# Performance work log

Hardware: AMD Instinct MI355X
Metric: run time of the kernel (lower is better)

## Reference

```python
import jax, jax.numpy as jnp
import numpy as np

EMB = 1024
HEADS = 16
B, N = 2, 2048

def setup_inputs() -> dict:
    key = jax.random.key(0)
    ks = jax.random.split(key, 9)
    s = 1.0 / np.sqrt(EMB)
    return {
        "x": jax.random.normal(ks[0], (B, N, EMB), dtype=jnp.float32),
        "Wq": jax.random.normal(ks[1], (EMB, EMB), dtype=jnp.float32) * s,
        "bq": jax.random.normal(ks[2], (EMB,), dtype=jnp.float32) * 0.01,
        "Wk": jax.random.normal(ks[3], (EMB, EMB), dtype=jnp.float32) * s,
        "bk": jax.random.normal(ks[4], (EMB,), dtype=jnp.float32) * 0.01,
        "Wv": jax.random.normal(ks[5], (EMB, EMB), dtype=jnp.float32) * s,
        "bv": jax.random.normal(ks[6], (EMB,), dtype=jnp.float32) * 0.01,
        "Wo": jax.random.normal(ks[7], (EMB, EMB), dtype=jnp.float32) * s,
        "bo": jax.random.normal(ks[8], (EMB,), dtype=jnp.float32) * 0.01,
    }

def _split_heads(t):
    b, n, e = t.shape
    return t.reshape(b, n, HEADS, e // HEADS).transpose(0, 2, 1, 3)  # b h n d

def reference(x, Wq, bq, Wk, bk, Wv, bv, Wo, bo):
    q = _split_heads(x @ Wq + bq)
    k = _split_heads(x @ Wk + bk)
    v = _split_heads(x @ Wv + bv)
    # NOTE: original scales by sqrt(emb_size), not sqrt(head_dim)
    scaling = jnp.asarray(EMB, x.dtype) ** 0.5
    energy = jnp.einsum('bhqd,bhkd->bhqk', q, k)
    att = jax.nn.softmax(energy / scaling, axis=-1)
    out = jnp.einsum('bhqk,bhkd->bhqd', att, v)
    out = out.transpose(0, 2, 1, 3).reshape(x.shape[0], x.shape[1], EMB)
    return out @ Wo + bo
```

## Files before the change

### kernel.cpp

```cpp
#include <hip/hip_runtime.h>
#include <hip/hip_bf16.h>

typedef __bf16 bf16_t;
typedef bf16_t bf16x8 __attribute__((ext_vector_type(8)));
typedef float f32x4 __attribute__((ext_vector_type(4)));
typedef float f32x2 __attribute__((ext_vector_type(2)));
typedef float f32x16 __attribute__((ext_vector_type(16)));

#define EMB 1024
#define HEADS 16
#define BATCH 2
#define SEQ 2048
#define HD 64
#define TOKENS (BATCH * SEQ)

__device__ __forceinline__ void gld16(bf16_t* lds_dst, const bf16_t* g_src) {
    __builtin_amdgcn_global_load_lds(
        (const __attribute__((address_space(1))) unsigned int*)g_src,
        (__attribute__((address_space(3))) unsigned int*)lds_dst, 16, 0, 0);
}

__device__ __forceinline__ unsigned cvt_pk_bf16(float lo, float hi) {
    unsigned r;
    asm("v_cvt_pk_bf16_f32 %0, %1, %2" : "=v"(r) : "v"(lo), "v"(hi));
    return r;
}

__device__ __forceinline__ float exp2_fast(float x) {
#if __has_builtin(__builtin_amdgcn_exp2f)
    return __builtin_amdgcn_exp2f(x);
#else
    return __expf(x * 0.69314718056f);
#endif
}

#define WAITV(N) asm volatile("s_waitcnt vmcnt(" #N ")" ::: "memory")
#define WAITLGKM() asm volatile("s_waitcnt lgkmcnt(0)" ::: "memory")
#define BAR() __builtin_amdgcn_s_barrier()

__global__ __launch_bounds__(256) void prep_all(
    const float* __restrict__ x, bf16_t* __restrict__ xb,
    const float* __restrict__ W0, const float* __restrict__ W1,
    const float* __restrict__ W2, const float* __restrict__ W3,
    bf16_t* __restrict__ T0, bf16_t* __restrict__ T1,
    bf16_t* __restrict__ T2, bf16_t* __restrict__ T3) {
    __shared__ __align__(16) bf16_t T[64][72];
    if (blockIdx.x < 1024) {
        size_t i = ((size_t)blockIdx.x * 256 + threadIdx.x) * 16;
        f32x4 v0 = *(const f32x4*)&x[i];
        f32x4 v1 = *(const f32x4*)&x[i + 4];
        f32x4 v2 = *(const f32x4*)&x[i + 8];
        f32x4 v3 = *(const f32x4*)&x[i + 12];
        bf16x8 o0, o1;
#pragma unroll
        for (int j = 0; j < 4; ++j) {
            o0[j] = (bf16_t)v0[j]; o0[4 + j] = (bf16_t)v1[j];
            o1[j] = (bf16_t)v2[j]; o1[4 + j] = (bf16_t)v3[j];
        }
        *(bf16x8*)&xb[i] = o0;
        *(bf16x8*)&xb[i + 8] = o1;
        return;
    }
    int t = blockIdx.x - 1024;
    int z = t >> 8, rid = t & 255;
    const float* src = (z == 0) ? W0 : (z == 1) ? W1 : (z == 2) ? W2 : W3;
    bf16_t* dst = (z == 0) ? T0 : (z == 1) ? T1 : (z == 2) ? T2 : T3;
    int k0 = (rid >> 4) * 64, n0 = (rid & 15) * 64;
    int r = threadIdx.x >> 2, c4 = (threadIdx.x & 3) * 16;
    f32x4 v[4];
#pragma unroll
    for (int q = 0; q < 4; ++q)
        v[q] = *(const f32x4*)&src[(size_t)(k0 + r) * 1024 + n0 + c4 + q * 4];
#pragma unroll
    for (int j = 0; j < 16; ++j) T[c4 + j][r] = (bf16_t)v[j >> 2][j & 3];
    __syncthreads();
    bf16x8 o0 = *(const bf16x8*)&T[r][c4];
    bf16x8 o1 = *(const bf16x8*)&T[r][c4 + 8];
    *(bf16x8*)&dst[(size_t)(n0 + r) * 1024 + k0 + c4] = o0;
    *(bf16x8*)&dst[(size_t)(n0 + r) * 1024 + k0 + c4 + 8] = o1;
}

template <typename TO>
__global__ __launch_bounds__(512) void gemm8p(
    const bf16_t* __restrict__ A, const bf16_t* __restrict__ W,
    const float* __restrict__ b0, const float* __restrict__ b1, const float* __restrict__ b2,
    TO* __restrict__ o0, TO* __restrict__ o1, TO* __restrict__ o2,
    int md0, int md1, int md2, float sc0, float sc1, float sc2,
    int XMP, int XNP, int CXM, int CXS) {
    __shared__ __align__(16) bf16_t As[2][256 * 64];
    __shared__ __align__(16) bf16_t Bs[2][256 * 64];

    const int tid = threadIdx.x, w = tid >> 6, lane = tid & 63;
    const int quad = lane >> 4, cc = lane & 15;
    const int wr = w >> 2, wc = w & 3;

    const int lin = blockIdx.x;
    const int xc = lin & 7, t = lin >> 3;
    const int mi = (xc & CXM) * XMP + (t % XMP);
    const int ni = (xc >> CXS) * XNP + (t / XMP);
    const int m0 = mi * 256, n0 = ni * 256;

    const int z = n0 >> 10;
    const float* bias = (z == 0) ? b0 : (z == 1) ? b1 : b2;
    TO* out = (z == 0) ? o0 : (z == 1) ? o1 : o2;
    const int mode = (z == 0) ? md0 : (z == 1) ? md1 : md2;
    const float scale = (z == 0) ? sc0 : (z == 1) ? sc1 : sc2;
    const int nz = n0 & 1023;

    f32x4 acc[8][4];
#pragma unroll
    for (int i = 0; i < 8; ++i)
#pragma unroll
        for (int j = 0; j < 4; ++j) acc[i][j] = (f32x4){0.f, 0.f, 0.f, 0.f};

    const int r8 = lane >> 3, sg = lane & 7;
    const int g8 = (sg ^ r8) * 8;
    const bf16_t* Ag = A + (size_t)m0 * 1024;
    const bf16_t* Bg = W + (size_t)n0 * 1024;

#define ST_A(BUF, TILE, H)                                                     \
    {                                                                          \
        _Pragma("unroll")                                                      \
        for (int s = 0; s < 2; ++s) {                                          \
            int rg = (H) * 128 + (w * 2 + s) * 8;                              \
            gld16(&As[BUF][rg * 64],                                           \
                  &Ag[(size_t)(rg + r8) * 1024 + (TILE) * 64 + g8]);           \
        }                                                                      \
    }
#define ST_B(BUF, TILE, H)                                                     \
    {                                                                          \
        _Pragma("unroll")                                                      \
        for (int s = 0; s < 2; ++s) {                                          \
            int rg = (H) * 128 + (w * 2 + s) * 8;                              \
            gld16(&Bs[BUF][rg * 64],                                           \
                  &Bg[(size_t)(rg + r8) * 1024 + (TILE) * 64 + g8]);           \
        }                                                                      \
    }

    const int soq = (quad ^ (cc & 7)) * 8;
    int rArow[8], rBrow[4];
#pragma unroll
    for (int mt = 0; mt < 8; ++mt) rArow[mt] = (wr * 128 + mt * 16 + cc) * 64;
#pragma unroll
    for (int nt = 0; nt < 4; ++nt) rBrow[nt] = (wc * 64 + nt * 16 + cc) * 64;

    bf16x8 bfr[4][2];
#define RD_B(BUF)                                                              \
    {                                                                          \
        _Pragma("unroll")                                                      \
        for (int nt = 0; nt < 4; ++nt) {                                       \
            bfr[nt][0] = *(const bf16x8*)&Bs[BUF][rBrow[nt] + soq];            \
            bfr[nt][1] = *(const bf16x8*)&Bs[BUF][rBrow[nt] + (soq ^ 32)];     \
        }                                                                      \
    }

#define PHASE(BUF, Q, STG)                                                     \
    {                                                                          \
        bf16x8 af0a = *(const bf16x8*)&As[BUF][rArow[(Q) * 2] + soq];          \
        bf16x8 af0b = *(const bf16x8*)&As[BUF][rArow[(Q) * 2] + (soq ^ 32)];   \
        bf16x8 af1a = *(const bf16x8*)&As[BUF][rArow[(Q) * 2 + 1] + soq];      \
        bf16x8 af1b = *(const bf16x8*)&As[BUF][rArow[(Q) * 2 + 1] + (soq ^ 32)]; \
        STG;                                                                   \
        WAITLGKM();                                                            \
        __builtin_amdgcn_sched_barrier(0);                                     \
        __builtin_amdgcn_s_setprio(1);                                         \
        _Pragma("unroll")                                                      \
        for (int nt = 0; nt < 4; ++nt) {                                       \
            acc[(Q) * 2][nt] = __builtin_amdgcn_mfma_f32_16x16x32_bf16(        \
                af0a, bfr[nt][0], acc[(Q) * 2][nt], 0, 0, 0);                  \
            acc[(Q) * 2][nt] = __builtin_amdgcn_mfma_f32_16x16x32_bf16(        \
                af0b, bfr[nt][1], acc[(Q) * 2][nt], 0, 0, 0);                  \
            acc[(Q) * 2 + 1][nt] = __builtin_amdgcn_mfma_f32_16x16x32_bf16(    \
                af1a, bfr[nt][0], acc[(Q) * 2 + 1][nt], 0, 0, 0);              \
            acc[(Q) * 2 + 1][nt] = __builtin_amdgcn_mfma_f32_16x16x32_bf16(    \
                af1b, bfr[nt][1], acc[(Q) * 2 + 1][nt], 0, 0, 0);              \
        }                                                                      \
        __builtin_amdgcn_s_setprio(0);                                         \
    }

    ST_A(0, 0, 0) ST_A(0, 0, 1) ST_B(0, 0, 0) ST_B(0, 0, 1)
    ST_B(1, 1, 0) ST_B(1, 1, 1)

    for (int i = 0; i < 8; ++i) {
        WAITV(4);
        BAR();
        RD_B(0)
        PHASE(0, 0, ST_A(1, 2 * i + 1, 0))
        BAR();
        PHASE(0, 1, ST_A(1, 2 * i + 1, 1))
        BAR();
        PHASE(0, 2, if (i < 7) ST_B(0, 2 * i + 2, 0))
        BAR();
        PHASE(0, 3, if (i < 7) ST_B(0, 2 * i + 2, 1))
        if (i < 7) { WAITV(4); } else { WAITV(0); }
        BAR();
        RD_B(1)
        PHASE(1, 0, if (i < 7) ST_A(0, 2 * i + 2, 0))
        BAR();
        PHASE(1, 1, if (i < 7) ST_A(0, 2 * i + 2, 1))
        BAR();
        PHASE(1, 2, if (i < 7) ST_B(1, 2 * i + 3, 0))
        BAR();
        PHASE(1, 3, if (i < 7) ST_B(1, 2 * i + 3, 1))
    }
#undef PHASE
#undef RD_B
#undef ST_A
#undef ST_B

    typedef TO TOx4 __attribute__((ext_vector_type(4)));
#pragma unroll
    for (int nt = 0; nt < 4; ++nt) {
        int colz = nz + wc * 64 + nt * 16 + cc;
        float bv = bias[colz];
#pragma unroll
        for (int mt = 0; mt < 8; ++mt) {
            if (mode == 2) {
                int row = m0 + wr * 128 + mt * 16 + quad * 4;
                int bb = row >> 11, n = row & 2047;
                int hh = colz >> 6, d = colz & 63;
                TOx4 pk;
#pragma unroll
                for (int r = 0; r < 4; ++r)
                    pk[r] = (TO)((acc[mt][nt][r] + bv) * scale);
                *(TOx4*)&out[((size_t)(bb * HEADS + hh) * HD + d) * SEQ + n] = pk;
            } else {
#pragma unroll
                for (int r = 0; r < 4; ++r) {
                    int row = m0 + wr * 128 + mt * 16 + quad * 4 + r;
                    float v = (acc[mt][nt][r] + bv) * scale;
                    size_t idx;
                    if (mode == 0) {
                        idx = (size_t)row * 1024 + colz;
                    } else {
                        int bb = row >> 11, n = row & 2047;
                        int hh = colz >> 6, d = colz & 63;
                        idx = ((size_t)(bb * HEADS + hh) * SEQ + n) * HD + d;
                    }
                    out[idx] = (TO)v;
                }
            }
        }
    }
}

template <typename TO>
__global__ __launch_bounds__(512) void gemm256(
    const bf16_t* __restrict__ A, const bf16_t* __restrict__ W,
    const float* __restrict__ b0, const float* __restrict__ b1, const float* __restrict__ b2,
    TO* __restrict__ o0, TO* __restrict__ o1, TO* __restrict__ o2,
    int md0, int md1, int md2, float sc0, float sc1, float sc2,
    int MP, int CM, int CSH, int NP) {
    __shared__ __align__(16) bf16_t As[3][256 * 64];
    __shared__ __align__(16) bf16_t Bs[3][128 * 64];

    const int tid = threadIdx.x, w = tid >> 6, lane = tid & 63;
    const int quad = lane >> 4, c = lane & 15;
    const int wm = (w >> 1) * 64, wn = (w & 1) * 64;

    const int lin = blockIdx.x;
    const int xc = lin & 7, t = lin >> 3;
    const int mi = MP * (xc & CM) + (t % MP);
    const int ni = NP * (xc >> CSH) + (t / MP);
    const int m0 = mi * 256, n0 = ni * 128;

    const int z = n0 >> 10;
    const float* bias = (z == 0) ? b0 : (z == 1) ? b1 : b2;
    TO* out = (z == 0) ? o0 : (z == 1) ? o1 : o2;
    const int mode = (z == 0) ? md0 : (z == 1) ? md1 : md2;
    const float scale = (z == 0) ? sc0 : (z == 1) ? sc1 : sc2;
    const int nz = n0 & 1023;

    f32x4 acc[4][4];
#pragma unroll
    for (int i = 0; i < 4; ++i)
#pragma unroll
        for (int j = 0; j < 4; ++j) acc[i][j] = (f32x4){0.f, 0.f, 0.f, 0.f};

    const int r8 = lane >> 3, sg = lane & 7;
    const int g8 = (sg ^ r8) * 8;
    const bf16_t* Ag = A + (size_t)m0 * 1024;
    const bf16_t* Bg = W + (size_t)n0 * 1024;
    int gA[4], lA[4], gB[2], lB[2];
#pragma unroll
    for (int s = 0; s < 4; ++s) {
        lA[s] = (w * 32 + s * 8) * 64;
        gA[s] = (w * 32 + s * 8 + r8) * 1024 + g8;
    }
#pragma unroll
    for (int s = 0; s < 2; ++s) {
        lB[s] = (w * 16 + s * 8) * 64;
        gB[s] = (w * 16 + s * 8 + r8) * 1024 + g8;
    }

    const int so = (quad ^ (c & 7)) * 8;
    int rA[4], rB[4];
#pragma unroll
    for (int i = 0; i < 4; ++i) {
        rA[i] = (wm + i * 16 + c) * 64;
        rB[i] = (wn + i * 16 + c) * 64;
    }

#define STAGE(BUF, T)                                                          \
    {                                                                          \
        int kn = (T) * 64;                                                     \
        _Pragma("unroll")                                                      \
        for (int s = 0; s < 4; ++s) gld16(&As[BUF][lA[s]], &Ag[gA[s] + kn]);   \
        _Pragma("unroll")                                                      \
        for (int s = 0; s < 2; ++s) gld16(&Bs[BUF][lB[s]], &Bg[gB[s] + kn]);   \
    }

#define FRAGS(CUR)                                                             \
    {                                                                          \
        _Pragma("unroll")                                                      \
        for (int ks = 0; ks < 2; ++ks) {                                       \
            int sk = so ^ (ks << 5);                                           \
            bf16x8 af[4], bfv[4];                                              \
            _Pragma("unroll")                                                  \
            for (int i = 0; i < 4; ++i)                                        \
                af[i] = *(const bf16x8*)&As[CUR][rA[i] + sk];                  \
            _Pragma("unroll")                                                  \
            for (int i = 0; i < 4; ++i)                                        \
                bfv[i] = *(const bf16x8*)&Bs[CUR][rB[i] + sk];                 \
            __builtin_amdgcn_s_setprio(1);                                     \
            _Pragma("unroll")                                                  \
            for (int mt = 0; mt < 4; ++mt)                                     \
                _Pragma("unroll")                                              \
                for (int nt = 0; nt < 4; ++nt)                                 \
                    acc[mt][nt] = __builtin_amdgcn_mfma_f32_16x16x32_bf16(     \
                        af[mt], bfv[nt], acc[mt][nt], 0, 0, 0);                \
            __builtin_amdgcn_s_setprio(0);                                     \
        }                                                                      \
    }

#define GSTEP(T, CUR)                                                          \
    {                                                                          \
        WAITV(6);                                                              \
        BAR();                                                                 \
        STAGE(((CUR) + 2) % 3, (T) + 2)                                        \
        FRAGS(CUR)                                                             \
    }

    STAGE(0, 0)
    STAGE(1, 1)
    for (int T = 0; T < 12; T += 3) {
        GSTEP(T, 0)
        GSTEP(T + 1, 1)
        GSTEP(T + 2, 2)
    }
    GSTEP(12, 0)
    GSTEP(13, 1)
    WAITV(6); BAR(); FRAGS(2)
    WAITV(0); BAR(); FRAGS(0)
#undef GSTEP
#undef FRAGS
#undef STAGE

    typedef TO TOx4 __attribute__((ext_vector_type(4)));
#pragma unroll
    for (int nt = 0; nt < 4; ++nt) {
        int colz = nz + wn + nt * 16 + c;
        float bv = bias[colz];
#pragma unroll
        for (int mt = 0; mt < 4; ++mt) {
            if (mode == 2) {
                int row = m0 + wm + mt * 16 + quad * 4;
                int bb = row >> 11, n = row & 2047;
                int hh = colz >> 6, d = colz & 63;
                TOx4 pk;
#pragma unroll
                for (int r = 0; r < 4; ++r)
                    pk[r] = (TO)((acc[mt][nt][r] + bv) * scale);
                *(TOx4*)&out[((size_t)(bb * HEADS + hh) * HD + d) * SEQ + n] = pk;
            } else {
#pragma unroll
                for (int r = 0; r < 4; ++r) {
                    int row = m0 + wm + mt * 16 + quad * 4 + r;
                    float v = (acc[mt][nt][r] + bv) * scale;
                    size_t idx;
                    if (mode == 0) {
                        idx = (size_t)row * 1024 + colz;
                    } else {
                        int bb = row >> 11, n = row & 2047;
                        int hh = colz >> 6, d = colz & 63;
                        idx = ((size_t)(bb * HEADS + hh) * SEQ + n) * HD + d;
                    }
                    out[idx] = (TO)v;
                }
            }
        }
    }
}

__global__ __launch_bounds__(256, 2) void attn_kernel(
    const bf16_t* __restrict__ Q, const bf16_t* __restrict__ K,
    const bf16_t* __restrict__ Vt, bf16_t* __restrict__ O) {
    __shared__ __align__(16) bf16_t Ks[2][2 * 64 * 64];
    __shared__ __align__(16) bf16_t Vs[2][2 * 64 * 64];

    const int tid = threadIdx.x, w = tid >> 6, lane = tid & 63;
    const int hi = lane >> 5, lq = lane & 31;

    const int lin = blockIdx.x + (blockIdx.y << 4);
    const int xcd = lin & 7, slot = lin >> 3;
    const int bh = xcd + ((slot >> 4) << 3);
    const int q0 = (slot & 15) << 7;
    const int b = bh >> 4, h = bh & 15;

    const int srow8 = lane >> 3, sch = lane & 7;

    const bf16_t* Kg0 = K + (size_t)bh * SEQ * HD;
    const bf16_t* Vg0 = Vt + (size_t)bh * HD * SEQ;

    int sl[2], sgK[2], sgV[2];
#pragma unroll
    for (int s = 0; s < 2; ++s) {
        int rg = (w * 2 + s) * 8;
        int row = rg + srow8;
        int g = sch ^ (row & 7);
        sl[s] = rg * 64;
        sgK[s] = row * 64 + g * 8;
        sgV[s] = row * SEQ + g * 8;
    }
    int rd[4];
#pragma unroll
    for (int dc = 0; dc < 4; ++dc)
        rd[dc] = lq * 64 + (((dc * 2 + hi) ^ (lq & 7)) * 8);

    bf16x8 qf[4];
    {
        const bf16_t* Qrow = Q + ((size_t)bh * SEQ + q0 + w * 32 + lq) * HD;
#pragma unroll
        for (int dc = 0; dc < 4; ++dc)
            qf[dc] = *(const bf16x8*)&Qrow[(dc * 2 + hi) * 8];
    }

#define STAGEPH(BUF, PH)                                                       \
    {                                                                          \
        const bf16_t* Kp = Kg0 + (size_t)(PH) * 128 * HD;                      \
        const bf16_t* Vp = Vg0 + (PH) * 128;                                   \
        _Pragma("unroll")                                                      \
        for (int s = 0; s < 2; ++s) {                                          \
            gld16(&Ks[BUF][sl[s]], &Kp[sgK[s]]);                               \
            gld16(&Ks[BUF][4096 + sl[s]], &Kp[4096 + sgK[s]]);                 \
            gld16(&Vs[BUF][sl[s]], &Vp[sgV[s]]);                               \
            gld16(&Vs[BUF][4096 + sl[s]], &Vp[64 + sgV[s]]);                   \
        }                                                                      \
    }

    STAGEPH(0, 0)

    f32x16 Zf;
#pragma unroll
    for (int r = 0; r < 16; ++r) Zf[r] = 0.f;

    f32x16 Oacc0, Oacc1;
#pragma unroll
    for (int r = 0; r < 16; ++r) { Oacc0[r] = 0.f; Oacc1[r] = 0.f; }
    f32x2 lpA = (f32x2){0.f, 0.f}, lpB = (f32x2){0.f, 0.f};

#define PACKFRAG(SS, c2, dstIdx)                                               \
        {                                                                      \
            unsigned pa = cvt_pk_bf16(SS[8 * (c2) + 0], SS[8 * (c2) + 1]);     \
            unsigned pb = cvt_pk_bf16(SS[8 * (c2) + 4], SS[8 * (c2) + 5]);     \
            unsigned pc = cvt_pk_bf16(SS[8 * (c2) + 2], SS[8 * (c2) + 3]);     \
            unsigned pd = cvt_pk_bf16(SS[8 * (c2) + 6], SS[8 * (c2) + 7]);     \
            asm volatile("v_permlane32_swap_b32 %0, %1" : "+v"(pa), "+v"(pb)); \
            asm volatile("v_permlane32_swap_b32 %0, %1" : "+v"(pc), "+v"(pd)); \
            union { unsigned u[4]; bf16x8 v; } pu;                             \
            pu.u[0] = pa; pu.u[1] = pc; pu.u[2] = pb; pu.u[3] = pd;            \
            pf[dstIdx] = pu.v;                                                 \
        }

#define MFMA32(A, B, C) __builtin_amdgcn_mfma_f32_32x32x16_bf16(A, B, C, 0, 0, 0)

#define ACORE2(BUF)                                                            \
    {                                                                          \
        f32x16 SA0, SA1, SB0, SB1;                                             \
        __builtin_amdgcn_s_setprio(1);                                         \
        {                                                                      \
            bf16x8 a0 = *(const bf16x8*)&Ks[BUF][rd[0]];                       \
            bf16x8 a1 = *(const bf16x8*)&Ks[BUF][rd[0] + 2048];                \
            bf16x8 b0 = *(const bf16x8*)&Ks[BUF][rd[0] + 4096];                \
            bf16x8 b1 = *(const bf16x8*)&Ks[BUF][rd[0] + 6144];                \
            SA0 = MFMA32(a0, qf[0], Zf);                                       \
            SA1 = MFMA32(a1, qf[0], Zf);                                       \
            SB0 = MFMA32(b0, qf[0], Zf);                                       \
            SB1 = MFMA32(b1, qf[0], Zf);                                       \
        }                                                                      \
        _Pragma("unroll")                                                      \
        for (int dc = 1; dc < 4; ++dc) {                                       \
            bf16x8 a0 = *(const bf16x8*)&Ks[BUF][rd[dc]];                      \
            bf16x8 a1 = *(const bf16x8*)&Ks[BUF][rd[dc] + 2048];               \
            bf16x8 b0 = *(const bf16x8*)&Ks[BUF][rd[dc] + 4096];               \
            bf16x8 b1 = *(const bf16x8*)&Ks[BUF][rd[dc] + 6144];               \
            SA0 = MFMA32(a0, qf[dc], SA0);                                     \
            SA1 = MFMA32(a1, qf[dc], SA1);                                     \
            SB0 = MFMA32(b0, qf[dc], SB0);                                     \
            SB1 = MFMA32(b1, qf[dc], SB1);                                     \
        }                                                                      \
        __builtin_amdgcn_s_setprio(0);                                         \
        _Pragma("unroll")                                                      \
        for (int r = 0; r < 16; r += 2) {                                      \
            SA0[r] = exp2_fast(SA0[r]); SA0[r + 1] = exp2_fast(SA0[r + 1]);    \
            lpA += (f32x2){SA0[r], SA0[r + 1]};                                \
            SA1[r] = exp2_fast(SA1[r]); SA1[r + 1] = exp2_fast(SA1[r + 1]);    \
            lpB += (f32x2){SA1[r], SA1[r + 1]};                                \
            SB0[r] = exp2_fast(SB0[r]); SB0[r + 1] = exp2_fast(SB0[r + 1]);    \
            lpA += (f32x2){SB0[r], SB0[r + 1]};                                \
            SB1[r] = exp2_fast(SB1[r]); SB1[r + 1] = exp2_fast(SB1[r + 1]);    \
            lpB += (f32x2){SB1[r], SB1[r + 1]};                                \
        }                                                                      \
        bf16x8 pf[8];                                                          \
        PACKFRAG(SA0, 0, 0) PACKFRAG(SA0, 1, 1)                                \
        PACKFRAG(SA1, 0, 2) PACKFRAG(SA1, 1, 3)                                \
        PACKFRAG(SB0, 0, 4) PACKFRAG(SB0, 1, 5)                                \
        PACKFRAG(SB1, 0, 6) PACKFRAG(SB1, 1, 7)                                \
        __builtin_amdgcn_s_setprio(1);                                         \
        _Pragma("unroll")                                                      \
        for (int f = 0; f < 4; ++f) {                                          \
            bf16x8 vA0 = *(const bf16x8*)&Vs[BUF][rd[f]];                      \
            bf16x8 vA1 = *(const bf16x8*)&Vs[BUF][rd[f] + 2048];               \
            bf16x8 vB0 = *(const bf16x8*)&Vs[BUF][rd[f] + 4096];               \
            bf16x8 vB1 = *(const bf16x8*)&Vs[BUF][rd[f] + 6144];               \
            Oacc0 = MFMA32(pf[f], vA0, Oacc0);                                 \
            Oacc1 = MFMA32(pf[f], vA1, Oacc1);                                 \
            Oacc0 = MFMA32(pf[4 + f], vB0, Oacc0);                             \
            Oacc1 = MFMA32(pf[4 + f], vB1, Oacc1);                             \
        }                                                                      \
        __builtin_amdgcn_s_setprio(0);                                         \
    }

    for (int p = 0; p < 16; p += 2) {
        WAITV(0);
        BAR();
        STAGEPH(1, p + 1)
        ACORE2(0)
        WAITV(0);
        BAR();
        if (p < 14) STAGEPH(0, p + 2)
        ACORE2(1)
    }
#undef ACORE2
#undef MFMA32
#undef PACKFRAG
#undef STAGEPH

    float lp = (lpA[0] + lpA[1]) + (lpB[0] + lpB[1]);
    lp += __shfl_xor(lp, 32);
    float rl = 1.0f / lp;

#pragma unroll
    for (int r = 0; r < 16; ++r) {
        int q_loc = (r & 3) + 8 * (r >> 2) + 4 * hi;
        float rr = __shfl(rl, q_loc);
        int qrow = q0 + w * 32 + q_loc;
        size_t base = ((size_t)(b * SEQ + qrow)) * EMB + h * 64;
        O[base + lq] = (bf16_t)(Oacc0[r] * rr);
        O[base + 32 + lq] = (bf16_t)(Oacc1[r] * rr);
    }
}

extern "C" void kernel_launch(void* const* d_in, const int* in_sizes, int n_in,
                              void* d_out, int out_size, void* d_ws, size_t ws_size,
                              hipStream_t stream) {
    (void)in_sizes; (void)n_in; (void)out_size; (void)ws_size;
    const float* x  = (const float*)d_in[0];
    const float* Wq = (const float*)d_in[1];
    const float* bq = (const float*)d_in[2];
    const float* Wk = (const float*)d_in[3];
    const float* bk = (const float*)d_in[4];
    const float* Wv = (const float*)d_in[5];
    const float* bv = (const float*)d_in[6];
    const float* Wo = (const float*)d_in[7];
    const float* bo = (const float*)d_in[8];

    bf16_t* ws = (bf16_t*)d_ws;
    const size_t NELEM = (size_t)TOKENS * EMB;
    const size_t WELEM = (size_t)EMB * EMB;
    bf16_t* Qb  = ws;
    bf16_t* Kb  = ws + NELEM;
    bf16_t* Vtb = ws + 2 * NELEM;
    bf16_t* Ob  = ws + 3 * NELEM;
    bf16_t* xb  = ws + 4 * NELEM;
    bf16_t* Wt0 = ws + 5 * NELEM;
    bf16_t* Wt1 = Wt0 + WELEM;
    bf16_t* Wt2 = Wt0 + 2 * WELEM;
    bf16_t* Wt3 = Wt0 + 3 * WELEM;
    (void)Wt1; (void)Wt2;

    hipLaunchKernelGGL(prep_all, dim3(2048), dim3(256), 0, stream,
                       x, xb, Wq, Wk, Wv, Wo, Wt0, Wt1, Wt2, Wt3);
    hipLaunchKernelGGL((gemm8p<bf16_t>), dim3(192), dim3(512), 0, stream,
                       xb, Wt0, bq, bk, bv, Qb, Kb, Vtb,
                       1, 1, 2, 0.0450842204f, 1.0f, 1.0f,
                       4, 6, 3, 2);
    hipLaunchKernelGGL(attn_kernel, dim3(16, 32), dim3(256), 0, stream, Qb, Kb, Vtb, Ob);
    hipLaunchKernelGGL((gemm256<float>), dim3(128), dim3(512), 0, stream,
                       Ob, Wt3, bo, bo, bo,
                       (float*)d_out, (float*)d_out, (float*)d_out,
                       0, 0, 0, 1.0f, 1.0f, 1.0f,
                       2, 7, 3, 8);
}
```

Baseline: 190.9 us.

## Process 64 query rows per wave in attention to reuse K/V tiles

Each attention wave now handles two 32-row query blocks instead of one, so every K and V fragment read from LDS feeds twice as many MFMAs. The block count halves (grid 8x32) and each block covers 256 queries, which halves the total K/V staging traffic. In exchange register pressure roughly doubles (launch bounds lowered to 1 block per CU) and fewer blocks are available to fill the GPU, which reduces occupancy and latency hiding.

```diff
diff --git a/kernel.cpp b/kernel.cpp
--- a/kernel.cpp
+++ b/kernel.cpp
@@ -392,7 +392,7 @@
     }
 }
 
-__global__ __launch_bounds__(256, 2) void attn_kernel(
+__global__ __launch_bounds__(256, 1) void attn_kernel(
     const bf16_t* __restrict__ Q, const bf16_t* __restrict__ K,
     const bf16_t* __restrict__ Vt, bf16_t* __restrict__ O) {
     __shared__ __align__(16) bf16_t Ks[2][2 * 64 * 64];
@@ -401,10 +401,10 @@
     const int tid = threadIdx.x, w = tid >> 6, lane = tid & 63;
     const int hi = lane >> 5, lq = lane & 31;
 
-    const int lin = blockIdx.x + (blockIdx.y << 4);
+    const int lin = blockIdx.x + (blockIdx.y << 3);
     const int xcd = lin & 7, slot = lin >> 3;
-    const int bh = xcd + ((slot >> 4) << 3);
-    const int q0 = (slot & 15) << 7;
+    const int bh = xcd + ((slot >> 3) << 3);
+    const int q0 = (slot & 7) << 8;
     const int b = bh >> 4, h = bh & 15;
 
     const int srow8 = lane >> 3, sch = lane & 7;
@@ -427,12 +427,15 @@
     for (int dc = 0; dc < 4; ++dc)
         rd[dc] = lq * 64 + (((dc * 2 + hi) ^ (lq & 7)) * 8);
 
-    bf16x8 qf[4];
+    bf16x8 qf0[4], qf1[4];
     {
-        const bf16_t* Qrow = Q + ((size_t)bh * SEQ + q0 + w * 32 + lq) * HD;
-#pragma unroll
-        for (int dc = 0; dc < 4; ++dc)
-            qf[dc] = *(const bf16x8*)&Qrow[(dc * 2 + hi) * 8];
+        const bf16_t* Qrow0 = Q + ((size_t)bh * SEQ + q0 + w * 64 + lq) * HD;
+        const bf16_t* Qrow1 = Qrow0 + 32 * HD;
+#pragma unroll
+        for (int dc = 0; dc < 4; ++dc) {
+            qf0[dc] = *(const bf16x8*)&Qrow0[(dc * 2 + hi) * 8];
+            qf1[dc] = *(const bf16x8*)&Qrow1[(dc * 2 + hi) * 8];
+        }
     }
 
 #define STAGEPH(BUF, PH)                                                       \
@@ -454,12 +457,13 @@
 #pragma unroll
     for (int r = 0; r < 16; ++r) Zf[r] = 0.f;
 
-    f32x16 Oacc0, Oacc1;
-#pragma unroll
-    for (int r = 0; r < 16; ++r) { Oacc0[r] = 0.f; Oacc1[r] = 0.f; }
-    f32x2 lpA = (f32x2){0.f, 0.f}, lpB = (f32x2){0.f, 0.f};
-
-#define PACKFRAG(SS, c2, dstIdx)                                               \
+    f32x16 O00, O01, O10, O11;
+#pragma unroll
+    for (int r = 0; r < 16; ++r) { O00[r] = 0.f; O01[r] = 0.f; O10[r] = 0.f; O11[r] = 0.f; }
+    f32x2 lp0a = (f32x2){0.f, 0.f}, lp0b = (f32x2){0.f, 0.f};
+    f32x2 lp1a = (f32x2){0.f, 0.f}, lp1b = (f32x2){0.f, 0.f};
+
+#define PACKFRAG(SS, c2, PF, dstIdx)                                           \
         {                                                                      \
             unsigned pa = cvt_pk_bf16(SS[8 * (c2) + 0], SS[8 * (c2) + 1]);     \
             unsigned pb = cvt_pk_bf16(SS[8 * (c2) + 4], SS[8 * (c2) + 5]);     \
@@ -469,24 +473,31 @@
             asm volatile("v_permlane32_swap_b32 %0, %1" : "+v"(pc), "+v"(pd)); \
             union { unsigned u[4]; bf16x8 v; } pu;                             \
             pu.u[0] = pa; pu.u[1] = pc; pu.u[2] = pb; pu.u[3] = pd;            \
-            pf[dstIdx] = pu.v;                                                 \
+            PF[dstIdx] = pu.v;                                                 \
         }
 
 #define MFMA32(A, B, C) __builtin_amdgcn_mfma_f32_32x32x16_bf16(A, B, C, 0, 0, 0)
 
+#define EXPLP(SS, LP)                                                          \
+        _Pragma("unroll")                                                      \
+        for (int r = 0; r < 16; r += 2) {                                      \
+            SS[r] = exp2_fast(SS[r]); SS[r + 1] = exp2_fast(SS[r + 1]);        \
+            LP += (f32x2){SS[r], SS[r + 1]};                                   \
+        }
+
 #define ACORE2(BUF)                                                            \
     {                                                                          \
-        f32x16 SA0, SA1, SB0, SB1;                                             \
+        f32x16 S0A0, S0A1, S0B0, S0B1, S1A0, S1A1, S1B0, S1B1;                 \
         __builtin_amdgcn_s_setprio(1);                                         \
         {                                                                      \
             bf16x8 a0 = *(const bf16x8*)&Ks[BUF][rd[0]];                       \
             bf16x8 a1 = *(const bf16x8*)&Ks[BUF][rd[0] + 2048];                \
             bf16x8 b0 = *(const bf16x8*)&Ks[BUF][rd[0] + 4096];                \
             bf16x8 b1 = *(const bf16x8*)&Ks[BUF][rd[0] + 6144];                \
-            SA0 = MFMA32(a0, qf[0], Zf);                                       \
-            SA1 = MFMA32(a1, qf[0], Zf);                                       \
-            SB0 = MFMA32(b0, qf[0], Zf);                                       \
-            SB1 = MFMA32(b1, qf[0], Zf);                                       \
+            S0A0 = MFMA32(a0, qf0[0], Zf); S0A1 = MFMA32(a1, qf0[0], Zf);      \
+            S0B0 = MFMA32(b0, qf0[0], Zf); S0B1 = MFMA32(b1, qf0[0], Zf);      \
+            S1A0 = MFMA32(a0, qf1[0], Zf); S1A1 = MFMA32(a1, qf1[0], Zf);      \
+            S1B0 = MFMA32(b0, qf1[0], Zf); S1B1 = MFMA32(b1, qf1[0], Zf);      \
         }                                                                      \
         _Pragma("unroll")                                                      \
         for (int dc = 1; dc < 4; ++dc) {                                       \
@@ -494,28 +505,23 @@
             bf16x8 a1 = *(const bf16x8*)&Ks[BUF][rd[dc] + 2048];               \
             bf16x8 b0 = *(const bf16x8*)&Ks[BUF][rd[dc] + 4096];               \
             bf16x8 b1 = *(const bf16x8*)&Ks[BUF][rd[dc] + 6144];               \
-            SA0 = MFMA32(a0, qf[dc], SA0);                                     \
-            SA1 = MFMA32(a1, qf[dc], SA1);                                     \
-            SB0 = MFMA32(b0, qf[dc], SB0);                                     \
-            SB1 = MFMA32(b1, qf[dc], SB1);                                     \
+            S0A0 = MFMA32(a0, qf0[dc], S0A0); S0A1 = MFMA32(a1, qf0[dc], S0A1); \
+            S0B0 = MFMA32(b0, qf0[dc], S0B0); S0B1 = MFMA32(b1, qf0[dc], S0B1); \
+            S1A0 = MFMA32(a0, qf1[dc], S1A0); S1A1 = MFMA32(a1, qf1[dc], S1A1); \
+            S1B0 = MFMA32(b0, qf1[dc], S1B0); S1B1 = MFMA32(b1, qf1[dc], S1B1); \
         }                                                                      \
         __builtin_amdgcn_s_setprio(0);                                         \
-        _Pragma("unroll")                                                      \
-        for (int r = 0; r < 16; r += 2) {                                      \
-            SA0[r] = exp2_fast(SA0[r]); SA0[r + 1] = exp2_fast(SA0[r + 1]);    \
-            lpA += (f32x2){SA0[r], SA0[r + 1]};                                \
-            SA1[r] = exp2_fast(SA1[r]); SA1[r + 1] = exp2_fast(SA1[r + 1]);    \
-            lpB += (f32x2){SA1[r], SA1[r + 1]};                                \
-            SB0[r] = exp2_fast(SB0[r]); SB0[r + 1] = exp2_fast(SB0[r + 1]);    \
-            lpA += (f32x2){SB0[r], SB0[r + 1]};                                \
-            SB1[r] = exp2_fast(SB1[r]); SB1[r + 1] = exp2_fast(SB1[r + 1]);    \
-            lpB += (f32x2){SB1[r], SB1[r + 1]};                                \
-        }                                                                      \
-        bf16x8 pf[8];                                                          \
-        PACKFRAG(SA0, 0, 0) PACKFRAG(SA0, 1, 1)                                \
-        PACKFRAG(SA1, 0, 2) PACKFRAG(SA1, 1, 3)                                \
-        PACKFRAG(SB0, 0, 4) PACKFRAG(SB0, 1, 5)                                \
-        PACKFRAG(SB1, 0, 6) PACKFRAG(SB1, 1, 7)                                \
+        EXPLP(S0A0, lp0a) EXPLP(S0A1, lp0b) EXPLP(S0B0, lp0a) EXPLP(S0B1, lp0b) \
+        EXPLP(S1A0, lp1a) EXPLP(S1A1, lp1b) EXPLP(S1B0, lp1a) EXPLP(S1B1, lp1b) \
+        bf16x8 pf0[8], pf1[8];                                                 \
+        PACKFRAG(S0A0, 0, pf0, 0) PACKFRAG(S0A0, 1, pf0, 1)                    \
+        PACKFRAG(S0A1, 0, pf0, 2) PACKFRAG(S0A1, 1, pf0, 3)                    \
+        PACKFRAG(S0B0, 0, pf0, 4) PACKFRAG(S0B0, 1, pf0, 5)                    \
+        PACKFRAG(S0B1, 0, pf0, 6) PACKFRAG(S0B1, 1, pf0, 7)                    \
+        PACKFRAG(S1A0, 0, pf1, 0) PACKFRAG(S1A0, 1, pf1, 1)                    \
+        PACKFRAG(S1A1, 0, pf1, 2) PACKFRAG(S1A1, 1, pf1, 3)                    \
+        PACKFRAG(S1B0, 0, pf1, 4) PACKFRAG(S1B0, 1, pf1, 5)                    \
+        PACKFRAG(S1B1, 0, pf1, 6) PACKFRAG(S1B1, 1, pf1, 7)                    \
         __builtin_amdgcn_s_setprio(1);                                         \
         _Pragma("unroll")                                                      \
         for (int f = 0; f < 4; ++f) {                                          \
@@ -523,10 +529,10 @@
             bf16x8 vA1 = *(const bf16x8*)&Vs[BUF][rd[f] + 2048];               \
             bf16x8 vB0 = *(const bf16x8*)&Vs[BUF][rd[f] + 4096];               \
             bf16x8 vB1 = *(const bf16x8*)&Vs[BUF][rd[f] + 6144];               \
-            Oacc0 = MFMA32(pf[f], vA0, Oacc0);                                 \
-            Oacc1 = MFMA32(pf[f], vA1, Oacc1);                                 \
-            Oacc0 = MFMA32(pf[4 + f], vB0, Oacc0);                             \
-            Oacc1 = MFMA32(pf[4 + f], vB1, Oacc1);                             \
+            O00 = MFMA32(pf0[f], vA0, O00); O01 = MFMA32(pf0[f], vA1, O01);    \
+            O10 = MFMA32(pf1[f], vA0, O10); O11 = MFMA32(pf1[f], vA1, O11);    \
+            O00 = MFMA32(pf0[4 + f], vB0, O00); O01 = MFMA32(pf0[4 + f], vB1, O01); \
+            O10 = MFMA32(pf1[4 + f], vB0, O10); O11 = MFMA32(pf1[4 + f], vB1, O11); \
         }                                                                      \
         __builtin_amdgcn_s_setprio(0);                                         \
     }
@@ -542,22 +548,29 @@
         ACORE2(1)
     }
 #undef ACORE2
+#undef EXPLP
 #undef MFMA32
 #undef PACKFRAG
 #undef STAGEPH
 
-    float lp = (lpA[0] + lpA[1]) + (lpB[0] + lpB[1]);
-    lp += __shfl_xor(lp, 32);
-    float rl = 1.0f / lp;
+    float lp0 = (lp0a[0] + lp0a[1]) + (lp0b[0] + lp0b[1]);
+    float lp1 = (lp1a[0] + lp1a[1]) + (lp1b[0] + lp1b[1]);
+    lp0 += __shfl_xor(lp0, 32);
+    lp1 += __shfl_xor(lp1, 32);
+    float rl0 = 1.0f / lp0, rl1 = 1.0f / lp1;
 
 #pragma unroll
     for (int r = 0; r < 16; ++r) {
         int q_loc = (r & 3) + 8 * (r >> 2) + 4 * hi;
-        float rr = __shfl(rl, q_loc);
-        int qrow = q0 + w * 32 + q_loc;
-        size_t base = ((size_t)(b * SEQ + qrow)) * EMB + h * 64;
-        O[base + lq] = (bf16_t)(Oacc0[r] * rr);
-        O[base + 32 + lq] = (bf16_t)(Oacc1[r] * rr);
+        float rr0 = __shfl(rl0, q_loc);
+        float rr1 = __shfl(rl1, q_loc);
+        int qrow0 = q0 + w * 64 + q_loc;
+        size_t base0 = ((size_t)(b * SEQ + qrow0)) * EMB + h * 64;
+        size_t base1 = base0 + (size_t)32 * EMB;
+        O[base0 + lq] = (bf16_t)(O00[r] * rr0);
+        O[base0 + 32 + lq] = (bf16_t)(O01[r] * rr0);
+        O[base1 + lq] = (bf16_t)(O10[r] * rr1);
+        O[base1 + 32 + lq] = (bf16_t)(O11[r] * rr1);
     }
 }
 
@@ -595,7 +608,7 @@
                        xb, Wt0, bq, bk, bv, Qb, Kb, Vtb,
                        1, 1, 2, 0.0450842204f, 1.0f, 1.0f,
                        4, 6, 3, 2);
-    hipLaunchKernelGGL(attn_kernel, dim3(16, 32), dim3(256), 0, stream, Qb, Kb, Vtb, Ob);
+    hipLaunchKernelGGL(attn_kernel, dim3(8, 32), dim3(256), 0, stream, Qb, Kb, Vtb, Ob);
     hipLaunchKernelGGL((gemm256<float>), dim3(128), dim3(512), 0, stream,
                        Ob, Wt3, bo, bo, bo,
                        (float*)d_out, (float*)d_out, (float*)d_out,
```

Result: slower. 196.7 us (+3.0%).

## Load K fragments directly from global into registers, keep only V in LDS

Applied to the files above, without the earlier changes.

K tiles no longer go through LDS. Each lane reads its MFMA K fragments straight from global memory into double-buffered register arrays, and the 128-key phase is split into two 64-key sub-steps. This halves LDS use and removes the LDS reads for K, but adds global-load latency on the critical path and uses more registers. The WAITV(0) waits now also cover the K register loads, so the overlap between loads and compute may shrink.

```diff
diff --git a/kernel.cpp b/kernel.cpp
--- a/kernel.cpp
+++ b/kernel.cpp
@@ -395,7 +395,6 @@
 __global__ __launch_bounds__(256, 2) void attn_kernel(
     const bf16_t* __restrict__ Q, const bf16_t* __restrict__ K,
     const bf16_t* __restrict__ Vt, bf16_t* __restrict__ O) {
-    __shared__ __align__(16) bf16_t Ks[2][2 * 64 * 64];
     __shared__ __align__(16) bf16_t Vs[2][2 * 64 * 64];
 
     const int tid = threadIdx.x, w = tid >> 6, lane = tid & 63;
@@ -412,14 +411,13 @@
     const bf16_t* Kg0 = K + (size_t)bh * SEQ * HD;
     const bf16_t* Vg0 = Vt + (size_t)bh * HD * SEQ;
 
-    int sl[2], sgK[2], sgV[2];
+    int sl[2], sgV[2];
 #pragma unroll
     for (int s = 0; s < 2; ++s) {
         int rg = (w * 2 + s) * 8;
         int row = rg + srow8;
         int g = sch ^ (row & 7);
         sl[s] = rg * 64;
-        sgK[s] = row * 64 + g * 8;
         sgV[s] = row * SEQ + g * 8;
     }
     int rd[4];
@@ -435,20 +433,31 @@
             qf[dc] = *(const bf16x8*)&Qrow[(dc * 2 + hi) * 8];
     }
 
-#define STAGEPH(BUF, PH)                                                       \
-    {                                                                          \
-        const bf16_t* Kp = Kg0 + (size_t)(PH) * 128 * HD;                      \
+    const bf16_t* Kl = Kg0 + (size_t)lq * HD + hi * 8;
+
+#define LDK(KF, T)                                                             \
+    {                                                                          \
+        const bf16_t* kp = Kl + (size_t)(T) * 64 * HD;                         \
+        _Pragma("unroll")                                                      \
+        for (int dc = 0; dc < 4; ++dc) {                                       \
+            KF[dc] = *(const bf16x8*)&kp[dc * 16];                             \
+            KF[4 + dc] = *(const bf16x8*)&kp[32 * HD + dc * 16];               \
+        }                                                                      \
+    }
+
+#define STAGEV(BUF, PH)                                                        \
+    {                                                                          \
         const bf16_t* Vp = Vg0 + (PH) * 128;                                   \
         _Pragma("unroll")                                                      \
         for (int s = 0; s < 2; ++s) {                                          \
-            gld16(&Ks[BUF][sl[s]], &Kp[sgK[s]]);                               \
-            gld16(&Ks[BUF][4096 + sl[s]], &Kp[4096 + sgK[s]]);                 \
             gld16(&Vs[BUF][sl[s]], &Vp[sgV[s]]);                               \
             gld16(&Vs[BUF][4096 + sl[s]], &Vp[64 + sgV[s]]);                   \
         }                                                                      \
     }
 
-    STAGEPH(0, 0)
+    bf16x8 kfA[8], kfB[8];
+    STAGEV(0, 0)
+    LDK(kfA, 0)
 
     f32x16 Zf;
 #pragma unroll
@@ -474,59 +483,35 @@
 
 #define MFMA32(A, B, C) __builtin_amdgcn_mfma_f32_32x32x16_bf16(A, B, C, 0, 0, 0)
 
-#define ACORE2(BUF)                                                            \
-    {                                                                          \
-        f32x16 SA0, SA1, SB0, SB1;                                             \
+#define TCORE(KF, BUF, VOFS)                                                   \
+    {                                                                          \
+        f32x16 S0, S1;                                                         \
         __builtin_amdgcn_s_setprio(1);                                         \
-        {                                                                      \
-            bf16x8 a0 = *(const bf16x8*)&Ks[BUF][rd[0]];                       \
-            bf16x8 a1 = *(const bf16x8*)&Ks[BUF][rd[0] + 2048];                \
-            bf16x8 b0 = *(const bf16x8*)&Ks[BUF][rd[0] + 4096];                \
-            bf16x8 b1 = *(const bf16x8*)&Ks[BUF][rd[0] + 6144];                \
-            SA0 = MFMA32(a0, qf[0], Zf);                                       \
-            SA1 = MFMA32(a1, qf[0], Zf);                                       \
-            SB0 = MFMA32(b0, qf[0], Zf);                                       \
-            SB1 = MFMA32(b1, qf[0], Zf);                                       \
-        }                                                                      \
+        S0 = MFMA32(KF[0], qf[0], Zf);                                         \
+        S1 = MFMA32(KF[4], qf[0], Zf);                                         \
         _Pragma("unroll")                                                      \
         for (int dc = 1; dc < 4; ++dc) {                                       \
-            bf16x8 a0 = *(const bf16x8*)&Ks[BUF][rd[dc]];                      \
-            bf16x8 a1 = *(const bf16x8*)&Ks[BUF][rd[dc] + 2048];               \
-            bf16x8 b0 = *(const bf16x8*)&Ks[BUF][rd[dc] + 4096];               \
-            bf16x8 b1 = *(const bf16x8*)&Ks[BUF][rd[dc] + 6144];               \
-            SA0 = MFMA32(a0, qf[dc], SA0);                                     \
-            SA1 = MFMA32(a1, qf[dc], SA1);                                     \
-            SB0 = MFMA32(b0, qf[dc], SB0);                                     \
-            SB1 = MFMA32(b1, qf[dc], SB1);                                     \
+            S0 = MFMA32(KF[dc], qf[dc], S0);                                   \
+            S1 = MFMA32(KF[4 + dc], qf[dc], S1);                               \
         }                                                                      \
         __builtin_amdgcn_s_setprio(0);                                         \
         _Pragma("unroll")                                                      \
         for (int r = 0; r < 16; r += 2) {                                      \
-            SA0[r] = exp2_fast(SA0[r]); SA0[r + 1] = exp2_fast(SA0[r + 1]);    \
-            lpA += (f32x2){SA0[r], SA0[r + 1]};                                \
-            SA1[r] = exp2_fast(SA1[r]); SA1[r + 1] = exp2_fast(SA1[r + 1]);    \
-            lpB += (f32x2){SA1[r], SA1[r + 1]};                                \
-            SB0[r] = exp2_fast(SB0[r]); SB0[r + 1] = exp2_fast(SB0[r + 1]);    \
-            lpA += (f32x2){SB0[r], SB0[r + 1]};                                \
-            SB1[r] = exp2_fast(SB1[r]); SB1[r + 1] = exp2_fast(SB1[r + 1]);    \
-            lpB += (f32x2){SB1[r], SB1[r + 1]};                                \
-        }                                                                      \
-        bf16x8 pf[8];                                                          \
-        PACKFRAG(SA0, 0, 0) PACKFRAG(SA0, 1, 1)                                \
-        PACKFRAG(SA1, 0, 2) PACKFRAG(SA1, 1, 3)                                \
-        PACKFRAG(SB0, 0, 4) PACKFRAG(SB0, 1, 5)                                \
-        PACKFRAG(SB1, 0, 6) PACKFRAG(SB1, 1, 7)                                \
+            S0[r] = exp2_fast(S0[r]); S0[r + 1] = exp2_fast(S0[r + 1]);        \
+            lpA += (f32x2){S0[r], S0[r + 1]};                                  \
+            S1[r] = exp2_fast(S1[r]); S1[r + 1] = exp2_fast(S1[r + 1]);        \
+            lpB += (f32x2){S1[r], S1[r + 1]};                                  \
+        }                                                                      \
+        bf16x8 pf[4];                                                          \
+        PACKFRAG(S0, 0, 0) PACKFRAG(S0, 1, 1)                                  \
+        PACKFRAG(S1, 0, 2) PACKFRAG(S1, 1, 3)                                  \
         __builtin_amdgcn_s_setprio(1);                                         \
         _Pragma("unroll")                                                      \
         for (int f = 0; f < 4; ++f) {                                          \
-            bf16x8 vA0 = *(const bf16x8*)&Vs[BUF][rd[f]];                      \
-            bf16x8 vA1 = *(const bf16x8*)&Vs[BUF][rd[f] + 2048];               \
-            bf16x8 vB0 = *(const bf16x8*)&Vs[BUF][rd[f] + 4096];               \
-            bf16x8 vB1 = *(const bf16x8*)&Vs[BUF][rd[f] + 6144];               \
-            Oacc0 = MFMA32(pf[f], vA0, Oacc0);                                 \
-            Oacc1 = MFMA32(pf[f], vA1, Oacc1);                                 \
-            Oacc0 = MFMA32(pf[4 + f], vB0, Oacc0);                             \
-            Oacc1 = MFMA32(pf[4 + f], vB1, Oacc1);                             \
+            bf16x8 v0 = *(const bf16x8*)&Vs[BUF][rd[f] + (VOFS)];              \
+            bf16x8 v1 = *(const bf16x8*)&Vs[BUF][rd[f] + 2048 + (VOFS)];       \
+            Oacc0 = MFMA32(pf[f], v0, Oacc0);                                  \
+            Oacc1 = MFMA32(pf[f], v1, Oacc1);                                  \
         }                                                                      \
         __builtin_amdgcn_s_setprio(0);                                         \
     }
@@ -534,17 +519,26 @@
     for (int p = 0; p < 16; p += 2) {
         WAITV(0);
         BAR();
-        STAGEPH(1, p + 1)
-        ACORE2(0)
+        STAGEV(1, p + 1)
+        LDK(kfB, 2 * p + 1)
+        TCORE(kfA, 0, 0)
         WAITV(0);
-        BAR();
-        if (p < 14) STAGEPH(0, p + 2)
-        ACORE2(1)
-    }
-#undef ACORE2
+        LDK(kfA, 2 * p + 2)
+        TCORE(kfB, 0, 4096)
+        WAITV(0);
+        BAR();
+        if (p < 14) STAGEV(0, p + 2)
+        LDK(kfB, 2 * p + 3)
+        TCORE(kfA, 1, 0)
+        WAITV(0);
+        if (p < 14) LDK(kfA, 2 * p + 4)
+        TCORE(kfB, 1, 4096)
+    }
+#undef TCORE
 #undef MFMA32
 #undef PACKFRAG
-#undef STAGEPH
+#undef STAGEV
+#undef LDK
 
     float lp = (lpA[0] + lpA[1]) + (lpB[0] + lpB[1]);
     lp += __shfl_xor(lp, 32);
```

New measurement: 216.2 us. 1.13x slower.
